# Optimization experiments

Measured on AMD Instinct MI355X. Metric: run time of the kernel, lower is better.

## Reference

```python
import jax, jax.numpy as jnp
import numpy as np
import math

B, N, IN_DIM, HID, HEADS, K, NCLS = 4, 8192, 1024, 512, 8, 16, 2


def setup_inputs() -> dict:
    key = jax.random.key(0)
    ks = jax.random.split(key, 20)
    s = 0.02
    return {
        "inputs": jax.random.normal(ks[0], (B, N, IN_DIM), jnp.float32),
        "W_feat": jax.random.normal(ks[1], (IN_DIM, HID), jnp.float32) * s,
        "b_feat": jnp.zeros((HID,), jnp.float32),
        "w_enc": jax.random.normal(ks[2], (HID, 1), jnp.float32) * s,
        "b_enc": jnp.zeros((1,), jnp.float32),
        "cls_token": jax.random.normal(ks[3], (1, 1, HID), jnp.float32) * s,
        "conv_w": jax.random.normal(ks[4], (HID, 1, 3, 3), jnp.float32) * s,  # depthwise
        "conv_b": jnp.zeros((HID,), jnp.float32),
        "Wq": jax.random.normal(ks[5], (HID, HID), jnp.float32) * s,
        "bq": jnp.zeros((HID,), jnp.float32),
        "Wk": jax.random.normal(ks[6], (HID, HID), jnp.float32) * s,
        "bk": jnp.zeros((HID,), jnp.float32),
        "Wv": jax.random.normal(ks[7], (HID, HID), jnp.float32) * s,
        "bv": jnp.zeros((HID,), jnp.float32),
        "Wo": jax.random.normal(ks[8], (HID, HID), jnp.float32) * s,
        "bo": jnp.zeros((HID,), jnp.float32),
        "Wc": jax.random.normal(ks[9], (HID, NCLS), jnp.float32) * s,
        "bc": jnp.zeros((NCLS,), jnp.float32),
    }


def reference(inputs, W_feat, b_feat, w_enc, b_enc, cls_token, conv_w, conv_b,
              Wq, bq, Wk, bk, Wv, bv, Wo, bo, Wc, bc):
    # ---- feature projection: [B,N,IN] -> [B,N,HID]
    x = inputs @ W_feat + b_feat

    # ---- recalib(option='max'): sigmoid scores, top-k gather, mean -> Q [B,1,HID]
    scores = jax.nn.sigmoid(jnp.squeeze(x @ w_enc + b_enc, -1))  # [B,N]
    _, idx = jax.lax.top_k(scores, K)                             # [B,K]
    topk = jnp.take_along_axis(x, idx[:, :, None], axis=1)        # [B,K,HID]
    Q = jnp.mean(topk, axis=1, keepdims=True)                     # [B,1,HID]

    # ---- shift + act
    x = jax.nn.relu(x - Q)

    # ---- pad to square grid and run depthwise 3x3 conv with residual
    _H = int(math.ceil(math.sqrt(N)))                             # 91
    add = _H * _H - N
    x = jnp.concatenate([x, x[:, :add]], axis=1)                  # [B, _H*_H, HID]
    feat = jnp.transpose(x, (0, 2, 1)).reshape(B, HID, _H, _H)    # [B,C,H,W]
    conv = jax.lax.conv_general_dilated(
        feat, conv_w, window_strides=(1, 1), padding="SAME",
        feature_group_count=HID)
    feat = conv + conv_b[None, :, None, None] + feat
    x = jnp.transpose(feat.reshape(B, HID, _H * _H), (0, 2, 1))   # [B,_H*_H,HID]

    # ---- prepend cls token
    cls = jnp.broadcast_to(cls_token, (B, 1, HID))
    x = jnp.concatenate([cls, x], axis=1)                         # [B,S,HID]

    # ---- MAB(Q, x): multi-head attention with scale 1/sqrt(dim_V)
    d = HID // HEADS
    q = (Q @ Wq + bq).reshape(B, 1, HEADS, d)
    kk = (x @ Wk + bk).reshape(B, -1, HEADS, d)
    v = (x @ Wv + bv).reshape(B, -1, HEADS, d)
    logits_a = jnp.einsum('bqhd,bkhd->bhqk', q, kk) / math.sqrt(HID)
    A = jax.nn.softmax(logits_a, axis=-1)                         # [B,h,1,S]
    O = q + jnp.einsum('bhqk,bkhd->bqhd', A, v)                   # [B,1,h,d]
    O = O.reshape(B, 1, HID)
    O = O + jax.nn.relu(O @ Wo + bo)
    bag = O[:, 0]                                                 # squeeze(1) -> [B,HID]

    return bag @ Wc + bc                                          # logits [B,NCLS]
```

## Files before the change

### kernel.cpp

```cpp
#include <hip/hip_runtime.h>
#include <math.h>

#define BB 4
#define NN 8192
#define IND 1024
#define HID 512
#define HEADS 8
#define KSEL 16
#define NCLS 2
#define HH 91
#define NPIX 8281
#define NTOK 8282
#define MROWS 32768

typedef short short8 __attribute__((ext_vector_type(8)));
typedef float floatx4 __attribute__((ext_vector_type(4)));

__device__ __forceinline__ unsigned short f2bf(float f) {
  union { float f; unsigned u; } v; v.f = f;
  unsigned r = (v.u + 0x7FFFu + ((v.u >> 16) & 1u)) >> 16;
  return (unsigned short)r;
}
__device__ __forceinline__ float bf2f(unsigned short h) {
  union { unsigned u; float f; } v; v.u = ((unsigned)h) << 16;
  return v.f;
}

__device__ __forceinline__ void gld16(const unsigned short* g, void* l) {
  typedef __attribute__((address_space(1))) const void GV;
  typedef __attribute__((address_space(3))) void LV;
  __builtin_amdgcn_global_load_lds((GV*)g, (LV*)l, 16, 0, 0);
}

__global__ void k_u(const float* __restrict__ W, const float* __restrict__ we,
                    float* __restrict__ u) {
  int wave = threadIdx.x >> 6, lane = threadIdx.x & 63;
  int k = blockIdx.x * 4 + wave;
  const float* wr = W + (long)k * HID + lane * 8;
  const float* wer = we + lane * 8;
  float a = 0.f;
#pragma unroll
  for (int i = 0; i < 8; ++i) a = fmaf(wr[i], wer[i], a);
  for (int off = 32; off; off >>= 1) a += __shfl_down(a, off);
  if (lane == 0) u[k] = a;
}

__global__ void k_wt(const float* __restrict__ W, unsigned short* __restrict__ Wt) {
  __shared__ unsigned short s[64][68];
  int kt = blockIdx.x * 64, nt = blockIdx.y * 64;
  int tid = threadIdx.x;
#pragma unroll
  for (int i = 0; i < 16; ++i) {
    int idx = tid + i * 256;
    int kk2 = idx >> 6, nn2 = idx & 63;
    s[nn2][kk2] = f2bf(W[(long)(kt + kk2) * HID + nt + nn2]);
  }
  __syncthreads();
#pragma unroll
  for (int i = 0; i < 16; ++i) {
    int idx = tid + i * 256;
    int nn2 = idx >> 6, kk2 = idx & 63;
    Wt[(long)(nt + nn2) * IND + kt + kk2] = s[nn2][kk2];
  }
}

__global__ void k_cvt(const float* __restrict__ in, const float* __restrict__ u,
                      unsigned short* __restrict__ abf, float* __restrict__ slog) {
  __shared__ float su[IND];
  int tid = threadIdx.x;
  for (int i = tid; i < IND; i += 256) su[i] = u[i];
  __syncthreads();
  int wave = tid >> 6, lane = tid & 63;
  long row = (long)blockIdx.x * 4 + wave;
  const float* ip = in + row * IND;
  unsigned short* op = abf + row * IND;
  float acc = 0.f;
#pragma unroll
  for (int p = 0; p < 4; ++p) {
    int k = p * 256 + lane * 4;
    float4 v = *(const float4*)(ip + k);
    ushort4 o;
    o.x = f2bf(v.x); o.y = f2bf(v.y); o.z = f2bf(v.z); o.w = f2bf(v.w);
    *(ushort4*)(op + k) = o;
    acc += v.x * su[k] + v.y * su[k + 1] + v.z * su[k + 2] + v.w * su[k + 3];
  }
  for (int off = 32; off; off >>= 1) acc += __shfl_down(acc, off);
  if (lane == 0) slog[row] = acc;
}

__global__ void k_gemm(const unsigned short* __restrict__ A,
                       const unsigned short* __restrict__ Bt,
                       const float* __restrict__ bias,
                       unsigned short* __restrict__ X) {
  __shared__ unsigned short sA[128 * 32];
  __shared__ unsigned short sB[128 * 32];
  int tid = threadIdx.x;
  int wave = tid >> 6, lane = tid & 63;
  long m0 = (long)blockIdx.x * 128;
  int n0 = blockIdx.y * 128;
  int wm = (wave >> 1) * 64, wn = (wave & 1) * 64;
  int lm = lane & 15, lk = (lane >> 4) * 8;
  floatx4 acc[4][4];
#pragma unroll
  for (int i = 0; i < 4; ++i)
#pragma unroll
    for (int j = 0; j < 4; ++j) acc[i][j] = (floatx4){0.f, 0.f, 0.f, 0.f};

  const unsigned short* gA = A + (m0 + (tid >> 2)) * IND + (tid & 3) * 8;
  const unsigned short* gB = Bt + (long)(n0 + (tid >> 2)) * IND + (tid & 3) * 8;
  char* sAc = (char*)sA + wave * 1024;
  char* sBc = (char*)sB + wave * 1024;

  for (int k0 = 0; k0 < IND; k0 += 32) {
    gld16(gA + k0, sAc);
    gld16(gA + k0 + 64 * IND, sAc + 4096);
    gld16(gB + k0, sBc);
    gld16(gB + k0 + 64 * IND, sBc + 4096);
    __syncthreads();
    short8 af[4], bfr[4];
#pragma unroll
    for (int i = 0; i < 4; ++i)
      af[i] = *(const short8*)(sA + (wm + i * 16 + lm) * 32 + lk);
#pragma unroll
    for (int j = 0; j < 4; ++j)
      bfr[j] = *(const short8*)(sB + (wn + j * 16 + lm) * 32 + lk);
#pragma unroll
    for (int i = 0; i < 4; ++i)
#pragma unroll
      for (int j = 0; j < 4; ++j)
        acc[i][j] = __builtin_amdgcn_mfma_f32_16x16x32_bf16(af[i], bfr[j], acc[i][j], 0, 0, 0);
    __syncthreads();
  }
#pragma unroll
  for (int j = 0; j < 4; ++j) {
    int gcol = n0 + wn + j * 16 + lm;
    float bv_ = bias[gcol];
#pragma unroll
    for (int i = 0; i < 4; ++i) {
      long grow = m0 + wm + i * 16 + (lane >> 4) * 4;
#pragma unroll
      for (int r = 0; r < 4; ++r)
        X[(grow + r) * HID + gcol] = f2bf(acc[i][j][r] + bv_);
    }
  }
}

__global__ void k_topq(const float* __restrict__ slog, const unsigned short* __restrict__ X,
                       float* __restrict__ Q) {
  __shared__ float sc[NN];
  __shared__ float rv[256];
  __shared__ int ri[256];
  __shared__ int wi[KSEL];
  int b = blockIdx.x, tid = threadIdx.x;
  for (int i = tid; i < NN; i += 256) sc[i] = slog[b * NN + i];
  __syncthreads();
  for (int it = 0; it < KSEL; ++it) {
    float bv = -3.4e38f; int bi = 0x7FFFFFFF;
    for (int i = tid; i < NN; i += 256) {
      float v = sc[i];
      if (v > bv) { bv = v; bi = i; }
    }
    rv[tid] = bv; ri[tid] = bi;
    __syncthreads();
    for (int s = 128; s; s >>= 1) {
      if (tid < s) {
        float v2 = rv[tid + s]; int i2 = ri[tid + s];
        if (v2 > rv[tid] || (v2 == rv[tid] && i2 < ri[tid])) { rv[tid] = v2; ri[tid] = i2; }
      }
      __syncthreads();
    }
    if (tid == 0) { wi[it] = ri[0]; sc[ri[0]] = -3.4e38f; }
    __syncthreads();
  }
  for (int c = tid; c < HID; c += 256) {
    float s = 0.f;
    for (int t2 = 0; t2 < KSEL; ++t2)
      s += bf2f(X[((long)b * NN + wi[t2]) * HID + c]);
    Q[b * HID + c] = s * (1.f / KSEL);
  }
}

__global__ void k_conv(const unsigned short* __restrict__ X, const float* __restrict__ Q,
                       const float* __restrict__ cw, const float* __restrict__ cb,
                       unsigned short* __restrict__ XT) {
  int tid = threadIdx.x;
  int b = blockIdx.y;
  int c = tid * 2;
  float w0[9], w1[9];
#pragma unroll
  for (int t = 0; t < 9; ++t) { w0[t] = cw[c * 9 + t]; w1[t] = cw[(c + 1) * 9 + t]; }
  float q0 = Q[b * HID + c], q1 = Q[b * HID + c + 1];
  float cb0 = cb[c], cb1 = cb[c + 1];
  int nbase = blockIdx.x * 8;
  const unsigned short* xb = X + (long)b * NN * HID;
#pragma unroll
  for (int ii = 0; ii < 8; ++ii) {
    int n = nbase + ii;
    if (n >= NPIX) break;
    int h = n / HH, w = n - h * HH;
    float a0 = 0.f, a1 = 0.f, c0v = 0.f, c1v = 0.f;
#pragma unroll
    for (int dy = 0; dy < 3; ++dy) {
      int hh2 = h + dy - 1;
      if (hh2 < 0 || hh2 >= HH) continue;
#pragma unroll
      for (int dx = 0; dx < 3; ++dx) {
        int ww2 = w + dx - 1;
        if (ww2 < 0 || ww2 >= HH) continue;
        int n2 = hh2 * HH + ww2;
        int r = n2 < NN ? n2 : n2 - NN;
        unsigned v = *(const unsigned*)(xb + (long)r * HID + c);
        float f0 = bf2f((unsigned short)(v & 0xFFFF));
        float f1 = bf2f((unsigned short)(v >> 16));
        f0 = fmaxf(f0 - q0, 0.f);
        f1 = fmaxf(f1 - q1, 0.f);
        int t = dy * 3 + dx;
        a0 = fmaf(w0[t], f0, a0);
        a1 = fmaf(w1[t], f1, a1);
        if (t == 4) { c0v = f0; c1v = f1; }
      }
    }
    unsigned out = (unsigned)f2bf(a0 + cb0 + c0v) | ((unsigned)f2bf(a1 + cb1 + c1v) << 16);
    *(unsigned*)(XT + ((long)b * NTOK + 1 + n) * HID + c) = out;
  }
}

__global__ void k_qv(const float* __restrict__ Q, const float* __restrict__ Wq,
                     const float* __restrict__ bq, const float* __restrict__ cls,
                     float* __restrict__ qvec, unsigned short* __restrict__ XT) {
  __shared__ float sq[HID];
  __shared__ float part[4][64];
  int b = blockIdx.y, cblk = blockIdx.x, tid = threadIdx.x;
  for (int i = tid; i < HID; i += 256) sq[i] = Q[b * HID + i];
  __syncthreads();
  int cl = tid & 63, seg = tid >> 6;
  int c = cblk * 64 + cl;
  float a = 0.f;
#pragma unroll 8
  for (int j = seg * 128; j < seg * 128 + 128; ++j)
    a = fmaf(sq[j], Wq[(long)j * HID + c], a);
  part[seg][cl] = a;
  __syncthreads();
  if (seg == 0)
    qvec[b * HID + c] = part[0][cl] + part[1][cl] + part[2][cl] + part[3][cl] + bq[c];
  if (cblk == 0)
    for (int i = tid; i < HID; i += 256)
      XT[(long)b * NTOK * HID + i] = f2bf(cls[i]);
}

__global__ void k_tprep(const float* __restrict__ qvec, const float* __restrict__ Wk,
                        const float* __restrict__ bk, float* __restrict__ tmat,
                        float* __restrict__ bkq) {
  __shared__ float qh[64];
  int b = blockIdx.y, h = blockIdx.x, tid = threadIdx.x;
  if (tid < 64) qh[tid] = qvec[b * HID + h * 64 + tid];
  __syncthreads();
  int d = tid & 63, jg = tid >> 6;
  float qd = qh[d];
  for (int jj = 0; jj < 128; ++jj) {
    int j = jj * 4 + jg;
    float v = Wk[(long)j * HID + h * 64 + d] * qd;
    for (int off = 32; off; off >>= 1) v += __shfl_down(v, off);
    if (d == 0) tmat[((long)b * HEADS + h) * HID + j] = v;
  }
  if (tid < 64) {
    float v = bk[h * 64 + tid] * qh[tid];
    for (int off = 32; off; off >>= 1) v += __shfl_down(v, off);
    if (tid == 0) bkq[b * HEADS + h] = v;
  }
}

__global__ void k_logits(const unsigned short* __restrict__ XT, const float* __restrict__ tmat,
                         const float* __restrict__ bkq, float* __restrict__ logits) {
  __shared__ float st[HEADS * HID];
  __shared__ float sb[HEADS];
  int b = blockIdx.y, tid = threadIdx.x;
  for (int i = tid; i < HEADS * HID; i += 256) st[i] = tmat[(long)b * HEADS * HID + i];
  if (tid < HEADS) sb[tid] = bkq[b * HEADS + tid];
  __syncthreads();
  int wave = tid >> 6, lane = tid & 63;
  float tr[HEADS][8];
#pragma unroll
  for (int h = 0; h < HEADS; ++h)
#pragma unroll
    for (int i = 0; i < 8; ++i) tr[h][i] = st[h * HID + lane * 8 + i];
  float sbr[HEADS];
#pragma unroll
  for (int h = 0; h < HEADS; ++h) sbr[h] = sb[h];

  for (long row = blockIdx.x * 4 + wave; row < NTOK; row += 4L * gridDim.x) {
    const unsigned short* xr = XT + ((long)b * NTOK + row) * HID + lane * 8;
    ushort4 v0 = *(const ushort4*)xr;
    ushort4 v1 = *(const ushort4*)(xr + 4);
    float xf[8] = {bf2f(v0.x), bf2f(v0.y), bf2f(v0.z), bf2f(v0.w),
                   bf2f(v1.x), bf2f(v1.y), bf2f(v1.z), bf2f(v1.w)};
    float acc[HEADS];
#pragma unroll
    for (int h = 0; h < HEADS; ++h) {
      float a = 0.f;
#pragma unroll
      for (int i = 0; i < 8; ++i) a = fmaf(xf[i], tr[h][i], a);
      acc[h] = a;
    }
#pragma unroll
    for (int h = 0; h < HEADS; ++h)
      for (int off = 32; off; off >>= 1) acc[h] += __shfl_down(acc[h], off);
    if (lane == 0) {
#pragma unroll
      for (int h = 0; h < HEADS; ++h)
        logits[((long)b * HEADS + h) * NTOK + row] = (acc[h] + sbr[h]) * 0.044194173824159216f;
    }
  }
}

__global__ void k_soft(float* __restrict__ logits) {
  __shared__ float sl[NTOK];
  __shared__ float red[256];
  int bh = blockIdx.x, tid = threadIdx.x;
  float* lp = logits + (long)bh * NTOK;
  for (int i = tid; i < NTOK; i += 256) sl[i] = lp[i];
  __syncthreads();
  float m = -3.4e38f;
  for (int i = tid; i < NTOK; i += 256) m = fmaxf(m, sl[i]);
  red[tid] = m; __syncthreads();
  for (int s = 128; s; s >>= 1) { if (tid < s) red[tid] = fmaxf(red[tid], red[tid + s]); __syncthreads(); }
  m = red[0]; __syncthreads();
  float sm = 0.f;
  for (int i = tid; i < NTOK; i += 256) {
    float e = __expf(sl[i] - m);
    sl[i] = e;
    sm += e;
  }
  red[tid] = sm; __syncthreads();
  for (int s = 128; s; s >>= 1) { if (tid < s) red[tid] += red[tid + s]; __syncthreads(); }
  float inv = 1.f / red[0];
  __syncthreads();
  for (int i = tid; i < NTOK; i += 256) lp[i] = sl[i] * inv;
}

__global__ void k_wsum(const unsigned short* __restrict__ XT, const float* __restrict__ P,
                       float* __restrict__ wsum) {
  __shared__ float pw[HEADS * 64];
  int b = blockIdx.y, tid = threadIdx.x;
  int nbase = blockIdx.x * 64;
  for (int i = tid; i < HEADS * 64; i += 256) {
    int h = i >> 6, nn = i & 63;
    long n = nbase + nn;
    pw[i] = (n < NTOK) ? P[((long)b * HEADS + h) * NTOK + n] : 0.f;
  }
  __syncthreads();
  int c = tid * 2;
  float wa[HEADS][2];
#pragma unroll
  for (int h = 0; h < HEADS; ++h) { wa[h][0] = 0.f; wa[h][1] = 0.f; }
  int lim = NTOK - nbase; if (lim > 64) lim = 64;
  for (int nn = 0; nn < lim; ++nn) {
    unsigned v = *(const unsigned*)(XT + ((long)b * NTOK + nbase + nn) * HID + c);
    float f0 = bf2f((unsigned short)(v & 0xFFFF));
    float f1 = bf2f((unsigned short)(v >> 16));
#pragma unroll
    for (int h = 0; h < HEADS; ++h) {
      float p = pw[h * 64 + nn];
      wa[h][0] = fmaf(p, f0, wa[h][0]);
      wa[h][1] = fmaf(p, f1, wa[h][1]);
    }
  }
#pragma unroll
  for (int h = 0; h < HEADS; ++h) {
    atomicAdd(&wsum[((long)b * HEADS + h) * HID + c], wa[h][0]);
    atomicAdd(&wsum[((long)b * HEADS + h) * HID + c + 1], wa[h][1]);
  }
}

__global__ void k_o1(const float* __restrict__ wsum, const float* __restrict__ Wv,
                     float* __restrict__ Opart) {
  __shared__ float part[2][128];
  int cblk = blockIdx.x, kc = blockIdx.y, b = blockIdx.z;
  int tid = threadIdx.x;
  int cl = tid & 127, seg = tid >> 7;
  int c = cblk * 128 + cl;
  int h = c >> 6;
  const float* wp = wsum + ((long)b * HEADS + h) * HID;
  int j0 = kc * 64 + seg * 32;
  float a = 0.f;
#pragma unroll 8
  for (int j = j0; j < j0 + 32; ++j) a = fmaf(wp[j], Wv[(long)j * HID + c], a);
  part[seg][cl] = a;
  __syncthreads();
  if (seg == 0) atomicAdd(&Opart[b * HID + c], part[0][cl] + part[1][cl]);
}

__global__ void k_o2a(const float* __restrict__ qvec, const float* __restrict__ bv,
                      const float* __restrict__ Opart, const float* __restrict__ Wo,
                      float* __restrict__ t2) {
  __shared__ float part[2][128];
  int cblk = blockIdx.x, kc = blockIdx.y, b = blockIdx.z;
  int tid = threadIdx.x;
  int cl = tid & 127, seg = tid >> 7;
  int c = cblk * 128 + cl;
  int j0 = kc * 64 + seg * 32;
  float a = 0.f;
#pragma unroll 8
  for (int j = j0; j < j0 + 32; ++j) {
    float so = qvec[b * HID + j] + bv[j] + Opart[b * HID + j];
    a = fmaf(so, Wo[(long)j * HID + c], a);
  }
  part[seg][cl] = a;
  __syncthreads();
  if (seg == 0) atomicAdd(&t2[b * HID + c], part[0][cl] + part[1][cl]);
}

__global__ void k_o2b(const float* __restrict__ qvec, const float* __restrict__ bv,
                      const float* __restrict__ Opart, const float* __restrict__ bo,
                      const float* __restrict__ t2, const float* __restrict__ Wc,
                      const float* __restrict__ bc, float* __restrict__ out) {
  __shared__ float r0[256], r1[256];
  int b = blockIdx.x, tid = threadIdx.x;
  float s0 = 0.f, s1 = 0.f;
  for (int c = tid; c < HID; c += 256) {
    float so = qvec[b * HID + c] + bv[c] + Opart[b * HID + c];
    float o2 = so + fmaxf(t2[b * HID + c] + bo[c], 0.f);
    s0 = fmaf(o2, Wc[c * 2], s0);
    s1 = fmaf(o2, Wc[c * 2 + 1], s1);
  }
  r0[tid] = s0; r1[tid] = s1;
  __syncthreads();
  for (int s = 128; s; s >>= 1) {
    if (tid < s) { r0[tid] += r0[tid + s]; r1[tid] += r1[tid + s]; }
    __syncthreads();
  }
  if (tid == 0) {
    out[b * NCLS + 0] = r0[0] + bc[0];
    out[b * NCLS + 1] = r1[0] + bc[1];
  }
}

extern "C" void kernel_launch(void* const* d_in, const int* in_sizes, int n_in,
                              void* d_out, int out_size, void* d_ws, size_t ws_size,
                              hipStream_t stream) {
  const float* inputs = (const float*)d_in[0];
  const float* W_feat = (const float*)d_in[1];
  const float* b_feat = (const float*)d_in[2];
  const float* w_enc  = (const float*)d_in[3];
  const float* cls    = (const float*)d_in[5];
  const float* conv_w = (const float*)d_in[6];
  const float* conv_b = (const float*)d_in[7];
  const float* Wq = (const float*)d_in[8];
  const float* bq = (const float*)d_in[9];
  const float* Wk = (const float*)d_in[10];
  const float* bk = (const float*)d_in[11];
  const float* Wv = (const float*)d_in[12];
  const float* bv = (const float*)d_in[13];
  const float* Wo = (const float*)d_in[14];
  const float* bo = (const float*)d_in[15];
  const float* Wc = (const float*)d_in[16];
  const float* bc = (const float*)d_in[17];
  float* out = (float*)d_out;

  char* ws = (char*)d_ws;
  size_t off = 0;
  auto alloc = [&](size_t bytes) -> void* {
    void* p = ws + off;
    off = (off + bytes + 255) & ~(size_t)255;
    return p;
  };
  unsigned short* abf = (unsigned short*)alloc((size_t)MROWS * IND * 2);
  unsigned short* wt  = (unsigned short*)alloc((size_t)HID * IND * 2);
  unsigned short* X   = (unsigned short*)alloc((size_t)MROWS * HID * 2);
  unsigned short* XT  = (unsigned short*)alloc((size_t)BB * NTOK * HID * 2);
  float* u      = (float*)alloc(IND * 4);
  float* slog   = (float*)alloc((size_t)MROWS * 4);
  float* Q      = (float*)alloc(BB * HID * 4);
  float* qvec   = (float*)alloc(BB * HID * 4);
  float* tmat   = (float*)alloc(BB * HEADS * HID * 4);
  float* bkq    = (float*)alloc(BB * HEADS * 4);
  float* logits = (float*)alloc((size_t)BB * HEADS * NTOK * 4);
  float* wsum   = (float*)alloc(BB * HEADS * HID * 4);
  float* Opart  = (float*)alloc(BB * HID * 4);
  float* t2buf  = (float*)alloc(BB * HID * 4);

  hipMemsetAsync(wsum, 0, BB * HEADS * HID * 4, stream);
  hipMemsetAsync(Opart, 0, BB * HID * 4, stream);
  hipMemsetAsync(t2buf, 0, BB * HID * 4, stream);

  k_u<<<IND / 4, 256, 0, stream>>>(W_feat, w_enc, u);
  k_wt<<<dim3(IND / 64, HID / 64), 256, 0, stream>>>(W_feat, wt);
  k_cvt<<<MROWS / 4, 256, 0, stream>>>(inputs, u, abf, slog);
  k_gemm<<<dim3(MROWS / 128, HID / 128), 256, 0, stream>>>(abf, wt, b_feat, X);
  k_topq<<<BB, 256, 0, stream>>>(slog, X, Q);
  k_conv<<<dim3((NPIX + 7) / 8, BB), 256, 0, stream>>>(X, Q, conv_w, conv_b, XT);
  k_qv<<<dim3(HID / 64, BB), 256, 0, stream>>>(Q, Wq, bq, cls, qvec, XT);
  k_tprep<<<dim3(HEADS, BB), 256, 0, stream>>>(qvec, Wk, bk, tmat, bkq);
  k_logits<<<dim3(132, BB), 256, 0, stream>>>(XT, tmat, bkq, logits);
  k_soft<<<BB * HEADS, 256, 0, stream>>>(logits);
  k_wsum<<<dim3((NTOK + 63) / 64, BB), 256, 0, stream>>>(XT, logits, wsum);
  k_o1<<<dim3(HID / 128, 8, BB), 256, 0, stream>>>(wsum, Wv, Opart);
  k_o2a<<<dim3(HID / 128, 8, BB), 256, 0, stream>>>(qvec, bv, Opart, Wo, t2buf);
  k_o2b<<<BB, 256, 0, stream>>>(qvec, bv, Opart, bo, t2buf, Wc, bc, out);
}
```

Baseline: 549.3 us.

## Widen GEMM tile, speed up top-k with wave shuffles, fuse small prep kernels

The feature GEMM now uses 512-thread blocks with a 128x256 output tile, so each A tile is loaded once per 256 output columns instead of per 128. Top-k selection runs with 1024 threads and wave-shuffle argmax reductions instead of a shared-memory tree with many barriers. The Q projection and key-transform prep kernels are merged into one kernel. The three memsets are folded into the softmax kernel to cut launches. The larger GEMM tile uses more LDS and threads per block, which may lower occupancy.

Result: no change. 540.4 us (-1.6%).

```diff
diff --git a/kernel.cpp b/kernel.cpp
--- a/kernel.cpp
+++ b/kernel.cpp
@@ -88,17 +88,17 @@
   if (lane == 0) slog[row] = acc;
 }
 
-__global__ void k_gemm(const unsigned short* __restrict__ A,
-                       const unsigned short* __restrict__ Bt,
-                       const float* __restrict__ bias,
-                       unsigned short* __restrict__ X) {
+__global__ __launch_bounds__(512) void k_gemm(const unsigned short* __restrict__ A,
+                                              const unsigned short* __restrict__ Bt,
+                                              const float* __restrict__ bias,
+                                              unsigned short* __restrict__ X) {
   __shared__ unsigned short sA[128 * 32];
-  __shared__ unsigned short sB[128 * 32];
+  __shared__ unsigned short sB[256 * 32];
   int tid = threadIdx.x;
   int wave = tid >> 6, lane = tid & 63;
   long m0 = (long)blockIdx.x * 128;
-  int n0 = blockIdx.y * 128;
-  int wm = (wave >> 1) * 64, wn = (wave & 1) * 64;
+  int n0 = blockIdx.y * 256;
+  int wm = (wave >> 2) * 64, wn = (wave & 3) * 64;
   int lm = lane & 15, lk = (lane >> 4) * 8;
   floatx4 acc[4][4];
 #pragma unroll
@@ -113,9 +113,8 @@
 
   for (int k0 = 0; k0 < IND; k0 += 32) {
     gld16(gA + k0, sAc);
-    gld16(gA + k0 + 64 * IND, sAc + 4096);
     gld16(gB + k0, sBc);
-    gld16(gB + k0 + 64 * IND, sBc + 4096);
+    gld16(gB + k0 + 128 * IND, sBc + 8192);
     __syncthreads();
     short8 af[4], bfr[4];
 #pragma unroll
@@ -145,38 +144,48 @@
   }
 }
 
-__global__ void k_topq(const float* __restrict__ slog, const unsigned short* __restrict__ X,
-                       float* __restrict__ Q) {
+__global__ __launch_bounds__(1024) void k_topq(const float* __restrict__ slog,
+                                               const unsigned short* __restrict__ X,
+                                               float* __restrict__ Q) {
   __shared__ float sc[NN];
-  __shared__ float rv[256];
-  __shared__ int ri[256];
+  __shared__ float wvs[16];
+  __shared__ int wis[16];
   __shared__ int wi[KSEL];
   int b = blockIdx.x, tid = threadIdx.x;
-  for (int i = tid; i < NN; i += 256) sc[i] = slog[b * NN + i];
+  int lane = tid & 63, wid = tid >> 6;
+  for (int i = tid; i < NN; i += 1024) sc[i] = slog[b * NN + i];
   __syncthreads();
   for (int it = 0; it < KSEL; ++it) {
     float bv = -3.4e38f; int bi = 0x7FFFFFFF;
-    for (int i = tid; i < NN; i += 256) {
+#pragma unroll
+    for (int r = 0; r < 8; ++r) {
+      int i = tid + r * 1024;
       float v = sc[i];
-      if (v > bv) { bv = v; bi = i; }
-    }
-    rv[tid] = bv; ri[tid] = bi;
+      if (v > bv || (v == bv && i < bi)) { bv = v; bi = i; }
+    }
+    for (int off = 32; off; off >>= 1) {
+      float v2 = __shfl_down(bv, off);
+      int i2 = __shfl_down(bi, off);
+      if (v2 > bv || (v2 == bv && i2 < bi)) { bv = v2; bi = i2; }
+    }
+    if (lane == 0) { wvs[wid] = bv; wis[wid] = bi; }
     __syncthreads();
-    for (int s = 128; s; s >>= 1) {
-      if (tid < s) {
-        float v2 = rv[tid + s]; int i2 = ri[tid + s];
-        if (v2 > rv[tid] || (v2 == rv[tid] && i2 < ri[tid])) { rv[tid] = v2; ri[tid] = i2; }
-      }
-      __syncthreads();
-    }
-    if (tid == 0) { wi[it] = ri[0]; sc[ri[0]] = -3.4e38f; }
+    if (tid == 0) {
+      float best = wvs[0]; int besti = wis[0];
+#pragma unroll
+      for (int w = 1; w < 16; ++w)
+        if (wvs[w] > best || (wvs[w] == best && wis[w] < besti)) { best = wvs[w]; besti = wis[w]; }
+      wi[it] = besti;
+      sc[besti] = -3.4e38f;
+    }
     __syncthreads();
   }
-  for (int c = tid; c < HID; c += 256) {
+  if (tid < HID) {
     float s = 0.f;
+#pragma unroll
     for (int t2 = 0; t2 < KSEL; ++t2)
-      s += bf2f(X[((long)b * NN + wi[t2]) * HID + c]);
-    Q[b * HID + c] = s * (1.f / KSEL);
+      s += bf2f(X[((long)b * NN + wi[t2]) * HID + tid]);
+    Q[b * HID + tid] = s * (1.f / KSEL);
   }
 }
 
@@ -225,35 +234,30 @@
   }
 }
 
-__global__ void k_qv(const float* __restrict__ Q, const float* __restrict__ Wq,
-                     const float* __restrict__ bq, const float* __restrict__ cls,
-                     float* __restrict__ qvec, unsigned short* __restrict__ XT) {
+__global__ void k_qkprep(const float* __restrict__ Q, const float* __restrict__ Wq,
+                         const float* __restrict__ bq, const float* __restrict__ Wk,
+                         const float* __restrict__ bk, const float* __restrict__ cls,
+                         float* __restrict__ qvec, float* __restrict__ tmat,
+                         float* __restrict__ bkq, unsigned short* __restrict__ XT) {
   __shared__ float sq[HID];
   __shared__ float part[4][64];
-  int b = blockIdx.y, cblk = blockIdx.x, tid = threadIdx.x;
+  __shared__ float qh[64];
+  int h = blockIdx.x, b = blockIdx.y, tid = threadIdx.x;
   for (int i = tid; i < HID; i += 256) sq[i] = Q[b * HID + i];
   __syncthreads();
   int cl = tid & 63, seg = tid >> 6;
-  int c = cblk * 64 + cl;
+  int c = h * 64 + cl;
   float a = 0.f;
 #pragma unroll 8
   for (int j = seg * 128; j < seg * 128 + 128; ++j)
     a = fmaf(sq[j], Wq[(long)j * HID + c], a);
   part[seg][cl] = a;
   __syncthreads();
-  if (seg == 0)
-    qvec[b * HID + c] = part[0][cl] + part[1][cl] + part[2][cl] + part[3][cl] + bq[c];
-  if (cblk == 0)
-    for (int i = tid; i < HID; i += 256)
-      XT[(long)b * NTOK * HID + i] = f2bf(cls[i]);
-}
-
-__global__ void k_tprep(const float* __restrict__ qvec, const float* __restrict__ Wk,
-                        const float* __restrict__ bk, float* __restrict__ tmat,
-                        float* __restrict__ bkq) {
-  __shared__ float qh[64];
-  int b = blockIdx.y, h = blockIdx.x, tid = threadIdx.x;
-  if (tid < 64) qh[tid] = qvec[b * HID + h * 64 + tid];
+  if (seg == 0) {
+    float q = part[0][cl] + part[1][cl] + part[2][cl] + part[3][cl] + bq[c];
+    qvec[b * HID + c] = q;
+    qh[cl] = q;
+  }
   __syncthreads();
   int d = tid & 63, jg = tid >> 6;
   float qd = qh[d];
@@ -268,6 +272,9 @@
     for (int off = 32; off; off >>= 1) v += __shfl_down(v, off);
     if (tid == 0) bkq[b * HEADS + h] = v;
   }
+  if (h == 0)
+    for (int i = tid; i < HID; i += 256)
+      XT[(long)b * NTOK * HID + i] = f2bf(cls[i]);
 }
 
 __global__ void k_logits(const unsigned short* __restrict__ XT, const float* __restrict__ tmat,
@@ -313,10 +320,17 @@
   }
 }
 
-__global__ void k_soft(float* __restrict__ logits) {
+__global__ void k_soft(float* __restrict__ logits, float* __restrict__ wsum,
+                       float* __restrict__ Opart, float* __restrict__ t2) {
   __shared__ float sl[NTOK];
   __shared__ float red[256];
   int bh = blockIdx.x, tid = threadIdx.x;
+  int b = bh >> 3, h = bh & 7;
+  for (int i = tid; i < HID; i += 256) wsum[(long)bh * HID + i] = 0.f;
+  if (tid < 64) {
+    Opart[b * HID + h * 64 + tid] = 0.f;
+    t2[b * HID + h * 64 + tid] = 0.f;
+  }
   float* lp = logits + (long)bh * NTOK;
   for (int i = tid; i < NTOK; i += 256) sl[i] = lp[i];
   __syncthreads();
@@ -479,20 +493,15 @@
   float* Opart  = (float*)alloc(BB * HID * 4);
   float* t2buf  = (float*)alloc(BB * HID * 4);
 
-  hipMemsetAsync(wsum, 0, BB * HEADS * HID * 4, stream);
-  hipMemsetAsync(Opart, 0, BB * HID * 4, stream);
-  hipMemsetAsync(t2buf, 0, BB * HID * 4, stream);
-
   k_u<<<IND / 4, 256, 0, stream>>>(W_feat, w_enc, u);
   k_wt<<<dim3(IND / 64, HID / 64), 256, 0, stream>>>(W_feat, wt);
   k_cvt<<<MROWS / 4, 256, 0, stream>>>(inputs, u, abf, slog);
-  k_gemm<<<dim3(MROWS / 128, HID / 128), 256, 0, stream>>>(abf, wt, b_feat, X);
-  k_topq<<<BB, 256, 0, stream>>>(slog, X, Q);
+  k_gemm<<<dim3(MROWS / 128, HID / 256), 512, 0, stream>>>(abf, wt, b_feat, X);
+  k_topq<<<BB, 1024, 0, stream>>>(slog, X, Q);
   k_conv<<<dim3((NPIX + 7) / 8, BB), 256, 0, stream>>>(X, Q, conv_w, conv_b, XT);
-  k_qv<<<dim3(HID / 64, BB), 256, 0, stream>>>(Q, Wq, bq, cls, qvec, XT);
-  k_tprep<<<dim3(HEADS, BB), 256, 0, stream>>>(qvec, Wk, bk, tmat, bkq);
+  k_qkprep<<<dim3(HEADS, BB), 256, 0, stream>>>(Q, Wq, bq, Wk, bk, cls, qvec, tmat, bkq, XT);
   k_logits<<<dim3(132, BB), 256, 0, stream>>>(XT, tmat, bkq, logits);
-  k_soft<<<BB * HEADS, 256, 0, stream>>>(logits);
+  k_soft<<<BB * HEADS, 256, 0, stream>>>(logits, wsum, Opart, t2buf);
   k_wsum<<<dim3((NTOK + 63) / 64, BB), 256, 0, stream>>>(XT, logits, wsum);
   k_o1<<<dim3(HID / 128, 8, BB), 256, 0, stream>>>(wsum, Wv, Opart);
   k_o2a<<<dim3(HID / 128, 8, BB), 256, 0, stream>>>(qvec, bv, Opart, Wo, t2buf);
```
